# Kernel tuning notes

Hardware: AMD Instinct MI355X
Metric: run time of the kernel (lower is better)

Reference implementation:

```python
import jax, jax.numpy as jnp
import numpy as np

N, E, IN, H, OUT, K = 50000, 800000, 128, 128, 40, 10
ALPHA, EPS, AH = 0.1, 1e-5, 64


def setup_inputs() -> dict:
    key = jax.random.key(0)
    ks = jax.random.split(key, 32)
    rn = lambda k, s, sc=0.05: jax.random.normal(k, s, jnp.float32) * sc
    return dict(
        x=jax.random.normal(ks[0], (N, IN), jnp.float32),
        edge_index=jax.random.randint(ks[1], (2, E), 0, N, jnp.int64),
        edge_weight=jax.random.uniform(ks[2], (E,), jnp.float32),
        lin1_w=rn(ks[3], (H, IN)), lin1_b=rn(ks[4], (H,)),
        bn1_g=jnp.ones((H,), jnp.float32), bn1_b=jnp.zeros((H,), jnp.float32),
        bn1_m=rn(ks[5], (H,)), bn1_v=jax.random.uniform(ks[6], (H,), jnp.float32, 0.5, 1.5),
        lin2_w=rn(ks[7], (H, H)), lin2_b=rn(ks[8], (H,)),
        bn2_g=jnp.ones((H,), jnp.float32), bn2_b=jnp.zeros((H,), jnp.float32),
        bn2_m=rn(ks[9], (H,)), bn2_v=jax.random.uniform(ks[10], (H,), jnp.float32, 0.5, 1.5),
        att1_w=rn(ks[11], (AH, 2 * H)), att1_b=rn(ks[12], (AH,)),
        att2_w=rn(ks[13], (K + 1, AH)), att2_b=rn(ks[14], (K + 1,)),
        head1_w=rn(ks[15], (H // 2, H)), head1_b=rn(ks[16], (H // 2,)),
        bn3_g=jnp.ones((H // 2,), jnp.float32), bn3_b=jnp.zeros((H // 2,), jnp.float32),
        bn3_m=rn(ks[17], (H // 2,)), bn3_v=jax.random.uniform(ks[18], (H // 2,), jnp.float32, 0.5, 1.5),
        head2_w=rn(ks[19], (OUT, H // 2)), head2_b=rn(ks[20], (OUT,)),
    )


def _bn(x, g, b, m, v):
    # eval-mode BatchNorm1d with running stats
    return (x - m) * jax.lax.rsqrt(v + EPS) * g + b


def reference(x, edge_index, edge_weight,
              lin1_w, lin1_b, bn1_g, bn1_b, bn1_m, bn1_v,
              lin2_w, lin2_b, bn2_g, bn2_b, bn2_m, bn2_v,
              att1_w, att1_b, att2_w, att2_b,
              head1_w, head1_b, bn3_g, bn3_b, bn3_m, bn3_v,
              head2_w, head2_b):
    row, col = edge_index[0], edge_index[1]

    # dense stem (dropout is identity in eval mode)
    h = jax.nn.relu(_bn(x @ lin1_w.T + lin1_b, bn1_g, bn1_b, bn1_m, bn1_v))
    identity = h
    h = jax.nn.relu(_bn(h @ lin2_w.T + lin2_b, bn2_g, bn2_b, bn2_m, bn2_v)) + identity
    base = h  # h0 for APPNP

    # edge normalization (loop-invariant): w_e / clamp(sum_w(row), 1)
    wsum = jnp.clip(jax.ops.segment_sum(edge_weight, row, num_segments=N), 1.0)
    enorm = edge_weight / wsum[row]  # [E]

    xs = [h]
    for _ in range(K):  # fixed K iterations of gather -> scatter-add
        agg = jax.ops.segment_sum(h[row] * enorm[:, None], col, num_segments=N)
        h = (1.0 - ALPHA) * agg + ALPHA * base
        xs.append(h)

    stacked = jnp.stack(xs, axis=-1)                    # [N, H, K+1]
    ctx = jnp.concatenate([xs[0], xs[-1]], axis=-1)     # [N, 2H]
    a = jax.nn.gelu(ctx @ att1_w.T + att1_b, approximate=False) @ att2_w.T + att2_b
    w = jax.nn.softmax(a, axis=-1)[:, None, :]          # [N, 1, K+1]
    fused = (stacked * w).sum(axis=-1)                  # [N, H]

    z = jax.nn.relu(_bn(fused @ head1_w.T + head1_b, bn3_g, bn3_b, bn3_m, bn3_v))
    return z @ head2_w.T + head2_b
```

## Files before the change

kernel.cpp:

```cpp
#include <hip/hip_runtime.h>
#include <hip/hip_fp16.h>
#include <math.h>

#define NN 50000
#define EE 800000
#define HH 128
#define KIT 10
#define NHF (NN * HH)
#define CC 64
#define CH 12500
#define RRH 4
#define NRH 12500

typedef _Float16 half8 __attribute__((ext_vector_type(8)));
typedef _Float16 half4v __attribute__((ext_vector_type(4)));
typedef float floatx4 __attribute__((ext_vector_type(4)));

static_assert(NN % 16 == 0, "row tiles must be exact");

__device__ __forceinline__ float gelu_exact(float x) {
  return 0.5f * x * (1.f + erff(x * 0.70710678118654752f));
}

__device__ __forceinline__ float4 ld4(const float* p) { return *(const float4*)p; }
__device__ __forceinline__ float4 ld4(const __half* p) {
  const __half2* q = (const __half2*)p;
  float2 lo = __half22float2(q[0]);
  float2 hi = __half22float2(q[1]);
  return make_float4(lo.x, lo.y, hi.x, hi.y);
}
__device__ __forceinline__ void st1(float* p, float v) { *p = v; }
__device__ __forceinline__ void st1(__half* p, float v) { *p = __float2half_rn(v); }

__global__ __launch_bounds__(256) void hist2_kernel(const int* __restrict__ ei,
                                                    const float* __restrict__ ew,
                                                    int* __restrict__ pdeg,
                                                    float* __restrict__ pwsum,
                                                    int* __restrict__ rank) {
  __shared__ int hist[NRH];
  const int c = blockIdx.x;
  const int z = blockIdx.y;
  const bool isdeg = (z < RRH);
  const int lo = (isdeg ? z : z - RRH) * NRH;
  for (int i = threadIdx.x; i < NRH; i += 256) hist[i] = 0;
  __syncthreads();
  const int e0 = c * CH;
  if (isdeg) {
    const int4* d4 = (const int4*)(ei + (size_t)EE + e0);
    for (int i = threadIdx.x; i < CH / 4; i += 256) {
      int4 d = d4[i];
      int e = e0 + i * 4;
      unsigned u0 = (unsigned)(d.x - lo), u1 = (unsigned)(d.y - lo);
      unsigned u2 = (unsigned)(d.z - lo), u3 = (unsigned)(d.w - lo);
      if (u0 < NRH) rank[e]     = atomicAdd(&hist[u0], 1);
      if (u1 < NRH) rank[e + 1] = atomicAdd(&hist[u1], 1);
      if (u2 < NRH) rank[e + 2] = atomicAdd(&hist[u2], 1);
      if (u3 < NRH) rank[e + 3] = atomicAdd(&hist[u3], 1);
    }
    __syncthreads();
    for (int i = threadIdx.x; i < NRH; i += 256)
      pdeg[(size_t)c * NN + lo + i] = hist[i];
  } else {
    float* whist = (float*)hist;
    const int4* s4 = (const int4*)(ei + e0);
    const float4* w4 = (const float4*)(ew + e0);
    for (int i = threadIdx.x; i < CH / 4; i += 256) {
      int4 s = s4[i];
      float4 w = w4[i];
      unsigned u0 = (unsigned)(s.x - lo), u1 = (unsigned)(s.y - lo);
      unsigned u2 = (unsigned)(s.z - lo), u3 = (unsigned)(s.w - lo);
      if (u0 < NRH) atomicAdd(&whist[u0], w.x);
      if (u1 < NRH) atomicAdd(&whist[u1], w.y);
      if (u2 < NRH) atomicAdd(&whist[u2], w.z);
      if (u3 < NRH) atomicAdd(&whist[u3], w.w);
    }
    __syncthreads();
    for (int i = threadIdx.x; i < NRH; i += 256)
      pwsum[(size_t)c * NN + lo + i] = whist[i];
  }
}

__global__ __launch_bounds__(256) void reduce_kernel(int* __restrict__ pdeg,
                                                     const float* __restrict__ pwsum,
                                                     int* __restrict__ deg,
                                                     float* __restrict__ wsum,
                                                     int* __restrict__ bsum) {
  int node = blockIdx.x * 256 + threadIdx.x;
  int acc = 0; float wacc = 0.f;
  if (node < NN) {
    for (int c = 0; c < CC; ++c) {
      size_t idx = (size_t)c * NN + node;
      int t = pdeg[idx];
      pdeg[idx] = acc;
      acc += t;
      wacc += pwsum[idx];
    }
    deg[node] = acc;
    wsum[node] = wacc;
  }
  __shared__ int red[256];
  red[threadIdx.x] = (node < NN) ? ((acc + 7) & ~7) : 0;
  __syncthreads();
  for (int off = 128; off > 0; off >>= 1) {
    if (threadIdx.x < off) red[threadIdx.x] += red[threadIdx.x + off];
    __syncthreads();
  }
  if (threadIdx.x == 0) bsum[blockIdx.x] = red[0];
}

__global__ __launch_bounds__(256) void scan2_kernel(const int* __restrict__ bsum,
                                                    int* __restrict__ boff,
                                                    int* __restrict__ row_start, int nb, int n) {
  __shared__ int buf[256];
  int tid = threadIdx.x;
  int v = (tid < nb) ? bsum[tid] : 0;
  buf[tid] = v;
  __syncthreads();
  for (int off = 1; off < 256; off <<= 1) {
    int t = (tid >= off) ? buf[tid - off] : 0;
    __syncthreads();
    buf[tid] += t;
    __syncthreads();
  }
  if (tid < nb) boff[tid] = buf[tid] - v;
  if (tid == 255) row_start[n] = buf[255];
}

__global__ __launch_bounds__(256) void scan3_kernel(const int* __restrict__ deg,
                                                    const int* __restrict__ boff,
                                                    int* __restrict__ row_start, int n) {
  __shared__ int buf[256];
  int tid = threadIdx.x;
  int i = blockIdx.x * 256 + tid;
  int v = (i < n) ? ((deg[i] + 7) & ~7) : 0;
  buf[tid] = v;
  __syncthreads();
  for (int off = 1; off < 256; off <<= 1) {
    int t = (tid >= off) ? buf[tid - off] : 0;
    __syncthreads();
    buf[tid] += t;
    __syncthreads();
  }
  if (i < n) row_start[i] = boff[blockIdx.x] + buf[tid] - v;
}

__global__ __launch_bounds__(256) void csr_fill_kernel(const int* __restrict__ ei,
                                                       const float* __restrict__ ew,
                                                       const float* __restrict__ wsum,
                                                       const int* __restrict__ row_start,
                                                       const int* __restrict__ pdeg_excl,
                                                       const int* __restrict__ rank,
                                                       int2* __restrict__ csr, int e_cnt) {
  int e = blockIdx.x * 256 + threadIdx.x;
  if (e >= e_cnt) return;
  int c = e / CH;
  int src = ei[e], dst = ei[EE + e];
  float ws = wsum[src];
  ws = ws < 1.f ? 1.f : ws;
  float v = 0.9f * ew[e] / ws;
  int pos = row_start[dst] + pdeg_excl[(size_t)c * NN + dst] + rank[e];
  csr[pos] = make_int2(src, __float_as_int(v));
}

__global__ __launch_bounds__(256) void pad_fill_kernel(const int* __restrict__ deg,
                                                       const int* __restrict__ row_start,
                                                       long* __restrict__ csr) {
  int node = blockIdx.x * 256 + threadIdx.x;
  if (node >= NN) return;
  int s = row_start[node] + deg[node];
  int e = row_start[node + 1];
  for (int i = s; i < e; ++i) csr[i] = 0;
}

__device__ __forceinline__ void prop_pair(int nA, int lane,
                                          const __half2* __restrict__ hc,
                                          const __half2* __restrict__ bp,
                                          const int* __restrict__ row_start,
                                          const long* __restrict__ csr,
                                          __half2* __restrict__ np) {
  int nB = nA + 1;
  float2 vbA = __half22float2(bp[(size_t)nA * 64 + lane]);
  float2 vbB = __half22float2(bp[(size_t)nB * 64 + lane]);
  float aAx = 0.1f * vbA.x, aAy = 0.1f * vbA.y, bAx = 0.f, bAy = 0.f;
  float aBx = 0.1f * vbB.x, aBy = 0.1f * vbB.y, bBx = 0.f, bBy = 0.f;
  int s  = __builtin_amdgcn_readfirstlane(row_start[nA]);
  int eA = __builtin_amdgcn_readfirstlane(row_start[nA + 1]);
  int eB = __builtin_amdgcn_readfirstlane(row_start[nB + 1]);
  int nb = (eB - s) >> 3;
  int i = s;
  if (nb > 0) {
    long cur[8];
    bool curB = (i >= eA);
#pragma unroll
    for (int j = 0; j < 8; ++j) cur[j] = csr[i + j];
    i += 8;
    for (int bidx = 1; bidx < nb; ++bidx) {
      long nxt[8];
      bool nxtB = (i >= eA);
#pragma unroll
      for (int j = 0; j < 8; ++j) nxt[j] = csr[i + j];
      i += 8;
      float2 g[8];
#pragma unroll
      for (int j = 0; j < 8; ++j) g[j] = __half22float2(hc[(size_t)(int)cur[j] * 64 + lane]);
      if (curB) {
#pragma unroll
        for (int j = 0; j < 8; ++j) {
          float v = __int_as_float((int)(cur[j] >> 32));
          if (j & 1) { bBx = fmaf(v, g[j].x, bBx); bBy = fmaf(v, g[j].y, bBy); }
          else       { aBx = fmaf(v, g[j].x, aBx); aBy = fmaf(v, g[j].y, aBy); }
        }
      } else {
#pragma unroll
        for (int j = 0; j < 8; ++j) {
          float v = __int_as_float((int)(cur[j] >> 32));
          if (j & 1) { bAx = fmaf(v, g[j].x, bAx); bAy = fmaf(v, g[j].y, bAy); }
          else       { aAx = fmaf(v, g[j].x, aAx); aAy = fmaf(v, g[j].y, aAy); }
        }
      }
#pragma unroll
      for (int j = 0; j < 8; ++j) cur[j] = nxt[j];
      curB = nxtB;
    }
    float2 g[8];
#pragma unroll
    for (int j = 0; j < 8; ++j) g[j] = __half22float2(hc[(size_t)(int)cur[j] * 64 + lane]);
    if (curB) {
#pragma unroll
      for (int j = 0; j < 8; ++j) {
        float v = __int_as_float((int)(cur[j] >> 32));
        if (j & 1) { bBx = fmaf(v, g[j].x, bBx); bBy = fmaf(v, g[j].y, bBy); }
        else       { aBx = fmaf(v, g[j].x, aBx); aBy = fmaf(v, g[j].y, aBy); }
      }
    } else {
#pragma unroll
      for (int j = 0; j < 8; ++j) {
        float v = __int_as_float((int)(cur[j] >> 32));
        if (j & 1) { bAx = fmaf(v, g[j].x, bAx); bAy = fmaf(v, g[j].y, bAy); }
        else       { aAx = fmaf(v, g[j].x, aAx); aAy = fmaf(v, g[j].y, aAy); }
      }
    }
  }
  np[(size_t)nA * 64 + lane] = __float22half2_rn(make_float2(aAx + bAx, aAy + bAy));
  np[(size_t)nB * 64 + lane] = __float22half2_rn(make_float2(aBx + bBx, aBy + bBy));
}

__global__ __launch_bounds__(256, 6) void prop_kernel(const __half* __restrict__ h_cur,
                                                      const __half* __restrict__ base,
                                                      const int* __restrict__ row_start,
                                                      const long* __restrict__ csr,
                                                      __half* __restrict__ h_next) {
  int pair = __builtin_amdgcn_readfirstlane((int)blockIdx.x * 4 + (int)(threadIdx.x >> 6));
  if (pair * 2 >= NN) return;
  prop_pair(pair * 2, threadIdx.x & 63, (const __half2*)h_cur, (const __half2*)base,
            row_start, csr, (__half2*)h_next);
}

template <int K, int KA, int JP, int JR, int ACT, bool RESID, typename IT, typename OT,
          bool ATT2 = false>
__global__ __launch_bounds__(256) void mfma_dense2(
    const IT* __restrict__ Xa, const IT* __restrict__ Xb,
    const float* __restrict__ W, const float* __restrict__ lb,
    const float* __restrict__ bg, const float* __restrict__ bb,
    const float* __restrict__ bm, const float* __restrict__ bv,
    const OT* __restrict__ resid, OT* __restrict__ out,
    const float* __restrict__ W2 = nullptr,
    const float* __restrict__ b2 = nullptr,
    float* __restrict__ attw_out = nullptr) {
  static_assert(K % 32 == 0 && KA % 32 == 0 && JP % 16 == 0, "");
  constexpr int JT = JP / 16;
  constexpr int NS = K / 32;
  constexpr bool ISF = __is_same(IT, float);
  __shared__ _Float16 wL[JP][K];
  static_assert(!ATT2 || (JP == 64 && JR == 64 && sizeof(wL) >= 64 * 65 * 4), "");

  const int tid = threadIdx.x;
  const int wv = tid >> 6, lane = tid & 63;
  const int q = lane >> 4, m = lane & 15;
  const int t = blockIdx.x * 4 + wv;
  const bool active = (t < NN / 16);
  const int row = t * 16 + m;

  half8  a[ISF ? 1 : NS];
  float4 af0[ISF ? NS : 1], af1[ISF ? NS : 1];
  if (active) {
#pragma unroll
    for (int s = 0; s < NS; ++s) {
      int c = s * 32 + q * 8;
      if constexpr (ISF) {
        const float* p = (const float*)Xa + (size_t)row * K + c;
        af0[s] = *(const float4*)p;
        af1[s] = *(const float4*)(p + 4);
      } else {
        const __half* p = (c < KA) ? (const __half*)Xa + (size_t)row * KA + c
                                   : (const __half*)Xb + (size_t)row * (K - KA) + (c - KA);
        a[s] = *(const half8*)p;
      }
    }
  }

  constexpr int C4 = K / 4;
  for (int idx = tid; idx < JP * C4; idx += 256) {
    int j = idx / C4;
    int c4 = (idx % C4) * 4;
    float4 v = make_float4(0.f, 0.f, 0.f, 0.f);
    if (j < JR) v = *(const float4*)&W[(size_t)j * K + c4];
    int cs = ((((c4 >> 3) ^ (j & 7)) << 3) | (c4 & 7));
    *(half4v*)&wL[j][cs] = (half4v){(_Float16)v.x, (_Float16)v.y,
                                    (_Float16)v.z, (_Float16)v.w};
  }
  __syncthreads();

  if constexpr (!ATT2) {
    if (!active) return;
  }

  floatx4 acc[JT];
#pragma unroll
  for (int jt = 0; jt < JT; ++jt) acc[jt] = (floatx4)(0.f);

  if (active) {
#pragma unroll
    for (int s = 0; s < NS; ++s) {
      half8 av;
      if constexpr (ISF) {
        float4 f0 = af0[s], f1 = af1[s];
        av = (half8){(_Float16)f0.x, (_Float16)f0.y, (_Float16)f0.z, (_Float16)f0.w,
                     (_Float16)f1.x, (_Float16)f1.y, (_Float16)f1.z, (_Float16)f1.w};
      } else {
        av = a[s];
      }
      int kq = s * 4 + q;
#pragma unroll
      for (int jt = 0; jt < JT; ++jt) {
        int j = jt * 16 + m;
        half8 b = *(const half8*)&wL[j][(kq ^ (j & 7)) << 3];
        acc[jt] = __builtin_amdgcn_mfma_f32_16x16x32_f16(av, b, acc[jt], 0, 0, 0);
      }
    }
  }

  if constexpr (ATT2) {
    float* attL = (float*)&wL[0][0];
    __syncthreads();
    if (active) {
#pragma unroll
      for (int jt = 0; jt < JT; ++jt) {
        int j = jt * 16 + m;
        float sh = lb[j];
#pragma unroll
        for (int reg = 0; reg < 4; ++reg) {
          float y = gelu_exact(acc[jt][reg] + sh);
          y = __half2float(__float2half_rn(y));
          attL[(wv * 16 + q * 4 + reg) * 65 + j] = y;
        }
      }
    }
    __syncthreads();
    if (tid < 64) {
      int n = blockIdx.x * 64 + tid;
      if (n < NN) {
        float a2[KIT + 1];
#pragma unroll
        for (int j = 0; j < KIT + 1; ++j) {
          float acc2 = b2[j];
#pragma unroll
          for (int k = 0; k < 64; ++k) acc2 = fmaf(attL[tid * 65 + k], W2[j * 64 + k], acc2);
          a2[j] = acc2;
        }
        float mx = a2[0];
#pragma unroll
        for (int j = 1; j < KIT + 1; ++j) mx = fmaxf(mx, a2[j]);
        float ssum = 0.f;
#pragma unroll
        for (int j = 0; j < KIT + 1; ++j) { a2[j] = expf(a2[j] - mx); ssum += a2[j]; }
        float inv = 1.f / ssum;
#pragma unroll
        for (int j = 0; j < KIT + 1; ++j) attw_out[n * 16 + j] = a2[j] * inv;
      }
    }
    return;
  }

#pragma unroll
  for (int jt = 0; jt < JT; ++jt) {
    int j = jt * 16 + m;
    if (j >= JR) continue;
    float sc = 0.f, sh;
    if (ACT == 1) {
      sc = bg[j] * rsqrtf(bv[j] + 1e-5f);
      sh = (lb[j] - bm[j]) * sc + bb[j];
    } else {
      sh = lb[j];
    }
#pragma unroll
    for (int reg = 0; reg < 4; ++reg) {
      int r = t * 16 + q * 4 + reg;
      float aa = acc[jt][reg];
      float y;
      if (ACT == 0)      y = aa + sh;
      else if (ACT == 1) y = fmaxf(fmaf(aa, sc, sh), 0.f);
      else               y = gelu_exact(aa + sh);
      if (RESID) y += (float)resid[(size_t)r * JR + j];
      st1(&out[(size_t)r * JR + j], y);
    }
  }
}

__global__ __launch_bounds__(256) void head1_fg_kernel(
    const __half* __restrict__ XS, const float* __restrict__ attw,
    const float* __restrict__ W, const float* __restrict__ lb,
    const float* __restrict__ bg, const float* __restrict__ bb,
    const float* __restrict__ bm, const float* __restrict__ bv,
    __half* __restrict__ out) {
  __shared__ _Float16 wL[64][128];
  __shared__ _Float16 fL[64][136];
  __shared__ float attL[64][16];
  const int tid = threadIdx.x;
  const int wv = tid >> 6, lane = tid & 63;
  const int q = lane >> 4, m = lane & 15;
  const int r0 = (int)blockIdx.x * 64;

  {
    int idx = tid * 4;
    int rr = idx >> 4;
    float4 v = make_float4(0.f, 0.f, 0.f, 0.f);
    if (r0 + rr < NN) v = *(const float4*)&attw[(size_t)(r0 + rr) * 16 + (idx & 15)];
    *(float4*)&attL[rr][idx & 15] = v;
  }
  for (int idx = tid; idx < 64 * 32; idx += 256) {
    int j = idx >> 5;
    int c4 = (idx & 31) * 4;
    float4 v = *(const float4*)&W[(size_t)j * 128 + c4];
    int cs = ((((c4 >> 3) ^ (j & 7)) << 3) | (c4 & 7));
    *(half4v*)&wL[j][cs] = (half4v){(_Float16)v.x, (_Float16)v.y,
                                    (_Float16)v.z, (_Float16)v.w};
  }
  __syncthreads();

  float f[4][8];
#pragma unroll
  for (int j = 0; j < 4; ++j)
#pragma unroll
    for (int e = 0; e < 8; ++e) f[j][e] = 0.f;
  const int trow = tid >> 4;
  const int tdim = (tid & 15) * 8;
  for (int k = 0; k <= KIT; ++k) {
    const __half* src = XS + (size_t)k * NHF + (size_t)r0 * 128;
    half8 v[4];
    float wk[4];
#pragma unroll
    for (int j = 0; j < 4; ++j) {
      int row = j * 16 + trow;
      if (r0 + row < NN) {
        v[j] = *(const half8*)(src + (size_t)row * 128 + tdim);
        wk[j] = attL[row][k];
      } else {
        v[j] = (half8)(_Float16)0.f;
        wk[j] = 0.f;
      }
    }
#pragma unroll
    for (int j = 0; j < 4; ++j)
#pragma unroll
      for (int e = 0; e < 8; ++e) f[j][e] = fmaf(wk[j], (float)v[j][e], f[j][e]);
  }
#pragma unroll
  for (int j = 0; j < 4; ++j) {
    int row = j * 16 + trow;
    half8 hv;
#pragma unroll
    for (int e = 0; e < 8; ++e) hv[e] = (_Float16)f[j][e];
    *(half8*)&fL[row][tdim] = hv;
  }
  __syncthreads();

  floatx4 acc[4];
#pragma unroll
  for (int jt = 0; jt < 4; ++jt) acc[jt] = (floatx4)(0.f);
#pragma unroll
  for (int s = 0; s < 4; ++s) {
    half8 av = *(const half8*)&fL[wv * 16 + m][s * 32 + q * 8];
    int kq = s * 4 + q;
#pragma unroll
    for (int jt = 0; jt < 4; ++jt) {
      int j = jt * 16 + m;
      half8 b = *(const half8*)&wL[j][(kq ^ (j & 7)) << 3];
      acc[jt] = __builtin_amdgcn_mfma_f32_16x16x32_f16(av, b, acc[jt], 0, 0, 0);
    }
  }
#pragma unroll
  for (int jt = 0; jt < 4; ++jt) {
    int j = jt * 16 + m;
    float sc = bg[j] * rsqrtf(bv[j] + 1e-5f);
    float sh = (lb[j] - bm[j]) * sc + bb[j];
#pragma unroll
    for (int reg = 0; reg < 4; ++reg) {
      int r = r0 + wv * 16 + q * 4 + reg;
      if (r < NN) {
        float y = fmaxf(fmaf(acc[jt][reg], sc, sh), 0.f);
        out[(size_t)r * 64 + j] = __float2half_rn(y);
      }
    }
  }
}

__global__ __launch_bounds__(256) void fused_accum_kernel(const __half* __restrict__ h,
                                                          const float* __restrict__ attw,
                                                          float* __restrict__ fused, int k) {
  int node = __builtin_amdgcn_readfirstlane((int)blockIdx.x * 4 + (int)(threadIdx.x >> 6));
  if (node >= NN) return;
  int lane = threadIdx.x & 63;
  float wk = attw[node * 16 + k];
  float2 v = __half22float2(((const __half2*)h)[(size_t)node * 64 + lane]);
  float2 o;
  if (k == 0) {
    o = make_float2(wk * v.x, wk * v.y);
  } else {
    float2 f = ((const float2*)fused)[(size_t)node * 64 + lane];
    o = make_float2(fmaf(wk, v.x, f.x), fmaf(wk, v.y, f.y));
  }
  ((float2*)fused)[(size_t)node * 64 + lane] = o;
}

extern "C" void kernel_launch(void* const* d_in, const int* in_sizes, int n_in,
                              void* d_out, int out_size, void* d_ws, size_t ws_size,
                              hipStream_t stream) {
  (void)in_sizes; (void)n_in; (void)out_size;
  const float* x      = (const float*)d_in[0];
  const int*   ei     = (const int*)d_in[1];
  const float* ew     = (const float*)d_in[2];
  const float* lin1_w = (const float*)d_in[3];
  const float* lin1_b = (const float*)d_in[4];
  const float* bn1_g  = (const float*)d_in[5];
  const float* bn1_b  = (const float*)d_in[6];
  const float* bn1_m  = (const float*)d_in[7];
  const float* bn1_v  = (const float*)d_in[8];
  const float* lin2_w = (const float*)d_in[9];
  const float* lin2_b = (const float*)d_in[10];
  const float* bn2_g  = (const float*)d_in[11];
  const float* bn2_b  = (const float*)d_in[12];
  const float* bn2_m  = (const float*)d_in[13];
  const float* bn2_v  = (const float*)d_in[14];
  const float* att1_w = (const float*)d_in[15];
  const float* att1_b = (const float*)d_in[16];
  const float* att2_w = (const float*)d_in[17];
  const float* att2_b = (const float*)d_in[18];
  const float* head1_w= (const float*)d_in[19];
  const float* head1_b= (const float*)d_in[20];
  const float* bn3_g  = (const float*)d_in[21];
  const float* bn3_b  = (const float*)d_in[22];
  const float* bn3_m  = (const float*)d_in[23];
  const float* bn3_v  = (const float*)d_in[24];
  const float* head2_w= (const float*)d_in[25];
  const float* head2_b= (const float*)d_in[26];
  float* out = (float*)d_out;

  char* p = (char*)d_ws;
  auto alloc = [&](size_t bytes) -> void* {
    void* r = (void*)p;
    p += (bytes + 255) & ~(size_t)255;
    return r;
  };
  int*   row_start= (int*)alloc((size_t)(NN + 1) * 4);
  int*   bsum     = (int*)alloc((size_t)256 * 4);
  int*   boff     = (int*)alloc((size_t)256 * 4);
  int*   deg      = (int*)alloc((size_t)NN * 4);
  float* wsum     = (float*)alloc((size_t)NN * 4);
  long*  csr      = (long*)alloc(((size_t)EE + 8 * NN) * 8);
  float* attw     = (float*)alloc((size_t)NN * 16 * 4);
  __half* h1      = (__half*)alloc((size_t)NHF * 2);
  __half* zbuf    = (__half*)alloc((size_t)NN * 64 * 2);
  size_t common = (size_t)(p - (char*)d_ws);
  size_t stored_need = common + (size_t)(KIT + 1) * NHF * 2 + 4096;
  bool stored = ws_size >= stored_need;

  __half* XS = nullptr;
  int* pdeg; float* pwsum; int* rank;
  if (stored) {
    XS = (__half*)alloc((size_t)(KIT + 1) * NHF * 2);
    char* ovl = (char*)(XS + (size_t)8 * NHF);
    pdeg  = (int*)ovl;
    pwsum = (float*)(ovl + (size_t)CC * NN * 4);
    rank  = (int*)(ovl + 2 * (size_t)CC * NN * 4);
  } else {
    pdeg  = (int*)alloc((size_t)CC * NN * 4);
    pwsum = (float*)alloc((size_t)CC * NN * 4);
    rank  = (int*)alloc((size_t)EE * 4);
  }

  const int GE  = (EE + 255) / 256;
  const int GN  = (NN + 255) / 256;
  const int GT  = (NN / 16 + 3) / 4;
  const int GP  = (NN + 3) / 4;
  const int GP2 = (NN / 2 + 3) / 4;

  hist2_kernel<<<dim3(CC, 2 * RRH), 256, 0, stream>>>(ei, ew, pdeg, pwsum, rank);
  reduce_kernel<<<GN, 256, 0, stream>>>(pdeg, pwsum, deg, wsum, bsum);
  scan2_kernel<<<1, 256, 0, stream>>>(bsum, boff, row_start, GN, NN);
  scan3_kernel<<<GN, 256, 0, stream>>>(deg, boff, row_start, NN);
  csr_fill_kernel<<<GE, 256, 0, stream>>>(ei, ew, wsum, row_start, pdeg, rank,
                                          (int2*)csr, EE);
  pad_fill_kernel<<<GN, 256, 0, stream>>>(deg, row_start, csr);

  if (stored) {
    mfma_dense2<128, 128, 128, 128, 1, false, float, __half><<<GT, 256, 0, stream>>>(
        x, (const float*)nullptr, lin1_w, lin1_b, bn1_g, bn1_b, bn1_m, bn1_v, nullptr, h1);
    mfma_dense2<128, 128, 128, 128, 1, true, __half, __half><<<GT, 256, 0, stream>>>(
        h1, (const __half*)nullptr, lin2_w, lin2_b, bn2_g, bn2_b, bn2_m, bn2_v, h1, XS);
    for (int k = 0; k < KIT; ++k) {
      prop_kernel<<<GP2, 256, 0, stream>>>(XS + (size_t)k * NHF, XS, row_start,
                                           csr, XS + (size_t)(k + 1) * NHF);
    }
    mfma_dense2<256, 128, 64, 64, 2, false, __half, __half, true>
        <<<GT, 256, 0, stream>>>(
        XS, XS + (size_t)KIT * NHF, att1_w, att1_b, nullptr, nullptr, nullptr, nullptr,
        nullptr, (__half*)nullptr, att2_w, att2_b, attw);
    head1_fg_kernel<<<GT, 256, 0, stream>>>(XS, attw, head1_w, head1_b,
                                            bn3_g, bn3_b, bn3_m, bn3_v, zbuf);
  } else {
    float*  fusedF = (float*)alloc((size_t)NHF * 4);
    __half* base   = (__half*)alloc((size_t)NHF * 2);
    __half* hA     = (__half*)alloc((size_t)NHF * 2);
    __half* hB     = (__half*)alloc((size_t)NHF * 2);
    mfma_dense2<128, 128, 128, 128, 1, false, float, __half><<<GT, 256, 0, stream>>>(
        x, (const float*)nullptr, lin1_w, lin1_b, bn1_g, bn1_b, bn1_m, bn1_v, nullptr, h1);
    mfma_dense2<128, 128, 128, 128, 1, true, __half, __half><<<GT, 256, 0, stream>>>(
        h1, (const __half*)nullptr, lin2_w, lin2_b, bn2_g, bn2_b, bn2_m, bn2_v, h1, base);
    const __half* cur = base;
    for (int k = 1; k <= KIT; ++k) {
      __half* nxt = (k & 1) ? hA : hB;
      prop_kernel<<<GP2, 256, 0, stream>>>(cur, base, row_start, csr, nxt);
      cur = nxt;
    }
    mfma_dense2<256, 128, 64, 64, 2, false, __half, __half, true>
        <<<GT, 256, 0, stream>>>(
        base, cur, att1_w, att1_b, nullptr, nullptr, nullptr, nullptr,
        nullptr, (__half*)nullptr, att2_w, att2_b, attw);
    fused_accum_kernel<<<GP, 256, 0, stream>>>(base, attw, fusedF, 0);
    cur = base;
    for (int k = 1; k <= KIT; ++k) {
      __half* nxt = (k & 1) ? hA : hB;
      prop_kernel<<<GP2, 256, 0, stream>>>(cur, base, row_start, csr, nxt);
      fused_accum_kernel<<<GP, 256, 0, stream>>>(nxt, attw, fusedF, k);
      cur = nxt;
    }
    mfma_dense2<128, 128, 64, 64, 1, false, float, __half><<<GT, 256, 0, stream>>>(
        fusedF, (const float*)nullptr, head1_w, head1_b, bn3_g, bn3_b, bn3_m, bn3_v,
        nullptr, zbuf);
  }

  mfma_dense2<64, 64, 48, 40, 0, false, __half, float><<<GT, 256, 0, stream>>>(
      zbuf, (const __half*)nullptr, head2_w, head2_b, nullptr, nullptr, nullptr, nullptr,
      nullptr, out);
}
```

Before: 542.6 us.

## Fuse lin1+lin2 stem and head1+head2 into single MFMA kernels

Replaces the two separate stem GEMM launches with one kernel that computes lin1+BN+ReLU, keeps the result in shared memory as fp16, then applies lin2+BN+ReLU plus the residual. It also extends the head kernel to run head2 directly from the shared-memory head1 output. This removes the h1 and zbuf global round-trips and two launches. In exchange it uses more shared memory per block, which may lower occupancy, and the residual is now read back from fp16 shared storage.

New measurement: 539.7 us. Within noise of the previous version (-0.5%).

```diff
diff --git a/kernel.cpp b/kernel.cpp
--- a/kernel.cpp
+++ b/kernel.cpp
@@ -407,12 +407,119 @@
   }
 }
 
-__global__ __launch_bounds__(256) void head1_fg_kernel(
+__global__ __launch_bounds__(256) void lin12_kernel(
+    const float* __restrict__ x,
+    const float* __restrict__ W1, const float* __restrict__ b1,
+    const float* __restrict__ g1, const float* __restrict__ be1,
+    const float* __restrict__ m1, const float* __restrict__ v1,
+    const float* __restrict__ W2, const float* __restrict__ b2,
+    const float* __restrict__ g2, const float* __restrict__ be2,
+    const float* __restrict__ m2, const float* __restrict__ v2,
+    __half* __restrict__ out) {
+  __shared__ _Float16 wL[128][128];
+  __shared__ _Float16 hL[64][136];
+  const int tid = threadIdx.x;
+  const int wv = tid >> 6, lane = tid & 63;
+  const int q = lane >> 4, m = lane & 15;
+  const int r0 = (int)blockIdx.x * 64;
+  const int row = r0 + wv * 16 + m;
+  const bool active = (row < NN);
+
+  float4 af0[4], af1[4];
+  if (active) {
+#pragma unroll
+    for (int s = 0; s < 4; ++s) {
+      const float* p = x + (size_t)row * 128 + s * 32 + q * 8;
+      af0[s] = *(const float4*)p;
+      af1[s] = *(const float4*)(p + 4);
+    }
+  }
+  for (int idx = tid; idx < 128 * 32; idx += 256) {
+    int j = idx >> 5;
+    int c4 = (idx & 31) * 4;
+    float4 v = *(const float4*)&W1[(size_t)j * 128 + c4];
+    int cs = ((((c4 >> 3) ^ (j & 7)) << 3) | (c4 & 7));
+    *(half4v*)&wL[j][cs] = (half4v){(_Float16)v.x, (_Float16)v.y,
+                                    (_Float16)v.z, (_Float16)v.w};
+  }
+  __syncthreads();
+
+  floatx4 acc1[8];
+#pragma unroll
+  for (int jt = 0; jt < 8; ++jt) acc1[jt] = (floatx4)(0.f);
+#pragma unroll
+  for (int s = 0; s < 4; ++s) {
+    float4 f0 = af0[s], f1 = af1[s];
+    half8 av = (half8){(_Float16)f0.x, (_Float16)f0.y, (_Float16)f0.z, (_Float16)f0.w,
+                       (_Float16)f1.x, (_Float16)f1.y, (_Float16)f1.z, (_Float16)f1.w};
+    int kq = s * 4 + q;
+#pragma unroll
+    for (int jt = 0; jt < 8; ++jt) {
+      int j = jt * 16 + m;
+      half8 b = *(const half8*)&wL[j][(kq ^ (j & 7)) << 3];
+      acc1[jt] = __builtin_amdgcn_mfma_f32_16x16x32_f16(av, b, acc1[jt], 0, 0, 0);
+    }
+  }
+  __syncthreads();
+
+#pragma unroll
+  for (int jt = 0; jt < 8; ++jt) {
+    int j = jt * 16 + m;
+    float sc = g1[j] * rsqrtf(v1[j] + 1e-5f);
+    float sh = (b1[j] - m1[j]) * sc + be1[j];
+#pragma unroll
+    for (int reg = 0; reg < 4; ++reg) {
+      float y = fmaxf(fmaf(acc1[jt][reg], sc, sh), 0.f);
+      hL[wv * 16 + q * 4 + reg][j] = (_Float16)y;
+    }
+  }
+  for (int idx = tid; idx < 128 * 32; idx += 256) {
+    int j = idx >> 5;
+    int c4 = (idx & 31) * 4;
+    float4 v = *(const float4*)&W2[(size_t)j * 128 + c4];
+    int cs = ((((c4 >> 3) ^ (j & 7)) << 3) | (c4 & 7));
+    *(half4v*)&wL[j][cs] = (half4v){(_Float16)v.x, (_Float16)v.y,
+                                    (_Float16)v.z, (_Float16)v.w};
+  }
+  __syncthreads();
+
+  floatx4 acc2[8];
+#pragma unroll
+  for (int jt = 0; jt < 8; ++jt) acc2[jt] = (floatx4)(0.f);
+#pragma unroll
+  for (int s = 0; s < 4; ++s) {
+    half8 av = *(const half8*)&hL[wv * 16 + m][s * 32 + q * 8];
+    int kq = s * 4 + q;
+#pragma unroll
+    for (int jt = 0; jt < 8; ++jt) {
+      int j = jt * 16 + m;
+      half8 b = *(const half8*)&wL[j][(kq ^ (j & 7)) << 3];
+      acc2[jt] = __builtin_amdgcn_mfma_f32_16x16x32_f16(av, b, acc2[jt], 0, 0, 0);
+    }
+  }
+  if (!active) return;
+#pragma unroll
+  for (int jt = 0; jt < 8; ++jt) {
+    int j = jt * 16 + m;
+    float sc = g2[j] * rsqrtf(v2[j] + 1e-5f);
+    float sh = (b2[j] - m2[j]) * sc + be2[j];
+#pragma unroll
+    for (int reg = 0; reg < 4; ++reg) {
+      int r = r0 + wv * 16 + q * 4 + reg;
+      float y = fmaxf(fmaf(acc2[jt][reg], sc, sh), 0.f);
+      y += (float)hL[wv * 16 + q * 4 + reg][j];
+      out[(size_t)r * 128 + j] = __float2half_rn(y);
+    }
+  }
+}
+
+__global__ __launch_bounds__(256) void head12_kernel(
     const __half* __restrict__ XS, const float* __restrict__ attw,
     const float* __restrict__ W, const float* __restrict__ lb,
     const float* __restrict__ bg, const float* __restrict__ bb,
     const float* __restrict__ bm, const float* __restrict__ bv,
-    __half* __restrict__ out) {
+    const float* __restrict__ W2, const float* __restrict__ lb2,
+    float* __restrict__ out) {
   __shared__ _Float16 wL[64][128];
   __shared__ _Float16 fL[64][136];
   __shared__ float attL[64][16];
@@ -489,6 +596,8 @@
       acc[jt] = __builtin_amdgcn_mfma_f32_16x16x32_f16(av, b, acc[jt], 0, 0, 0);
     }
   }
+  __syncthreads();
+
 #pragma unroll
   for (int jt = 0; jt < 4; ++jt) {
     int j = jt * 16 + m;
@@ -496,11 +605,44 @@
     float sh = (lb[j] - bm[j]) * sc + bb[j];
 #pragma unroll
     for (int reg = 0; reg < 4; ++reg) {
+      float y = fmaxf(fmaf(acc[jt][reg], sc, sh), 0.f);
+      fL[wv * 16 + q * 4 + reg][j] = (_Float16)y;
+    }
+  }
+  for (int idx = tid; idx < 48 * 16; idx += 256) {
+    int j = idx >> 4;
+    int c4 = (idx & 15) * 4;
+    float4 v = make_float4(0.f, 0.f, 0.f, 0.f);
+    if (j < 40) v = *(const float4*)&W2[(size_t)j * 64 + c4];
+    int cs = ((((c4 >> 3) ^ (j & 7)) << 3) | (c4 & 7));
+    *(half4v*)&wL[j][cs] = (half4v){(_Float16)v.x, (_Float16)v.y,
+                                    (_Float16)v.z, (_Float16)v.w};
+  }
+  __syncthreads();
+
+  floatx4 acc2[3];
+#pragma unroll
+  for (int jt = 0; jt < 3; ++jt) acc2[jt] = (floatx4)(0.f);
+#pragma unroll
+  for (int s = 0; s < 2; ++s) {
+    half8 av = *(const half8*)&fL[wv * 16 + m][s * 32 + q * 8];
+    int kq = s * 4 + q;
+#pragma unroll
+    for (int jt = 0; jt < 3; ++jt) {
+      int j = jt * 16 + m;
+      half8 b = *(const half8*)&wL[j][(kq ^ (j & 7)) << 3];
+      acc2[jt] = __builtin_amdgcn_mfma_f32_16x16x32_f16(av, b, acc2[jt], 0, 0, 0);
+    }
+  }
+#pragma unroll
+  for (int jt = 0; jt < 3; ++jt) {
+    int j = jt * 16 + m;
+    if (j >= 40) continue;
+    float sh = lb2[j];
+#pragma unroll
+    for (int reg = 0; reg < 4; ++reg) {
       int r = r0 + wv * 16 + q * 4 + reg;
-      if (r < NN) {
-        float y = fmaxf(fmaf(acc[jt][reg], sc, sh), 0.f);
-        out[(size_t)r * 64 + j] = __float2half_rn(y);
-      }
+      if (r < NN) out[(size_t)r * 40 + j] = acc2[jt][reg] + sh;
     }
   }
 }
@@ -604,10 +746,9 @@
   pad_fill_kernel<<<GN, 256, 0, stream>>>(deg, row_start, csr);
 
   if (stored) {
-    mfma_dense2<128, 128, 128, 128, 1, false, float, __half><<<GT, 256, 0, stream>>>(
-        x, (const float*)nullptr, lin1_w, lin1_b, bn1_g, bn1_b, bn1_m, bn1_v, nullptr, h1);
-    mfma_dense2<128, 128, 128, 128, 1, true, __half, __half><<<GT, 256, 0, stream>>>(
-        h1, (const __half*)nullptr, lin2_w, lin2_b, bn2_g, bn2_b, bn2_m, bn2_v, h1, XS);
+    lin12_kernel<<<GT, 256, 0, stream>>>(
+        x, lin1_w, lin1_b, bn1_g, bn1_b, bn1_m, bn1_v,
+        lin2_w, lin2_b, bn2_g, bn2_b, bn2_m, bn2_v, XS);
     for (int k = 0; k < KIT; ++k) {
       prop_kernel<<<GP2, 256, 0, stream>>>(XS + (size_t)k * NHF, XS, row_start,
                                            csr, XS + (size_t)(k + 1) * NHF);
@@ -616,8 +757,9 @@
         <<<GT, 256, 0, stream>>>(
         XS, XS + (size_t)KIT * NHF, att1_w, att1_b, nullptr, nullptr, nullptr, nullptr,
         nullptr, (__half*)nullptr, att2_w, att2_b, attw);
-    head1_fg_kernel<<<GT, 256, 0, stream>>>(XS, attw, head1_w, head1_b,
-                                            bn3_g, bn3_b, bn3_m, bn3_v, zbuf);
+    head12_kernel<<<GT, 256, 0, stream>>>(XS, attw, head1_w, head1_b,
+                                          bn3_g, bn3_b, bn3_m, bn3_v,
+                                          head2_w, head2_b, out);
   } else {
     float*  fusedF = (float*)alloc((size_t)NHF * 4);
     __half* base   = (__half*)alloc((size_t)NHF * 2);
@@ -648,9 +790,8 @@
     mfma_dense2<128, 128, 64, 64, 1, false, float, __half><<<GT, 256, 0, stream>>>(
         fusedF, (const float*)nullptr, head1_w, head1_b, bn3_g, bn3_b, bn3_m, bn3_v,
         nullptr, zbuf);
-  }
-
-  mfma_dense2<64, 64, 48, 40, 0, false, __half, float><<<GT, 256, 0, stream>>>(
-      zbuf, (const __half*)nullptr, head2_w, head2_b, nullptr, nullptr, nullptr, nullptr,
-      nullptr, out);
-}
+    mfma_dense2<64, 64, 48, 40, 0, false, __half, float><<<GT, 256, 0, stream>>>(
+        zbuf, (const __half*)nullptr, head2_w, head2_b, nullptr, nullptr, nullptr, nullptr,
+        nullptr, out);
+  }
+}
```
